# Optimization experiments

Hardware: AMD Instinct MI355X
Metric: run time of the kernel (lower is better)

## Reference

```python
import jax, jax.numpy as jnp
import numpy as np

ALPHA_LEAKY = 0.2
EPS = 1e-10


def setup_inputs() -> dict:
    key = jax.random.key(0)
    ks = jax.random.split(key, 7)
    Nq, Nk, E, D = 100000, 100000, 1600000, 64
    return {
        "query_nodes": jax.random.normal(ks[0], (Nq, D), dtype=jnp.float32),
        "key_value_nodes": jax.random.normal(ks[1], (Nk, D), dtype=jnp.float32),
        "edge_index": jax.random.randint(ks[2], (2, E), 0, Nq, dtype=jnp.int64),
        "proj_w": jax.random.normal(ks[3], (D, D), dtype=jnp.float32) * 0.1,
        "proj_b": jax.random.normal(ks[4], (D,), dtype=jnp.float32) * 0.1,
        "attend_w": jax.random.normal(ks[5], (1, 2 * D), dtype=jnp.float32) * 0.1,
        "attend_b": jax.random.normal(ks[6], (1,), dtype=jnp.float32) * 0.1,
    }


def reference(query_nodes, key_value_nodes, edge_index, proj_w, proj_b, attend_w, attend_b):
    Nq, D = query_nodes.shape
    qi, ki = edge_index[0], edge_index[1]  # [E], [E]
    # per-edge gathered + projected features (torch Linear: x @ W.T + b)
    query_proj = query_nodes[qi] @ proj_w.T + proj_b      # [E, D]
    kv_proj = key_value_nodes[ki] @ proj_w.T + proj_b     # [E, D]
    # attend(concat([qp, kp])) == qp @ Wq.T + kp @ Wk.T + b  (avoids [E,2D] concat)
    wq, wk = attend_w[:, :D], attend_w[:, D:]
    e = query_proj @ wq[0] + kv_proj @ wk[0] + attend_b[0]  # [E]
    e = jax.nn.leaky_relu(e, negative_slope=ALPHA_LEAKY)
    # segment-wise (per query node) numerically-stable softmax
    e_max = jax.ops.segment_max(e, qi, num_segments=Nq)    # [Nq] (-inf for empty)
    e_exp = jnp.exp(e - e_max[qi])                          # [E]
    e_sum = jax.ops.segment_sum(e_exp, qi, num_segments=Nq)  # [Nq]
    attention = e_exp / (e_sum[qi] + EPS)                   # [E]  (dropout = identity in eval)
    # weighted scatter-add aggregation back to query nodes
    weighted_values = kv_proj * attention[:, None]          # [E, D]
    aggregated_context = jax.ops.segment_sum(weighted_values, qi, num_segments=Nq)  # [Nq, D]
    return aggregated_context
```

## Files before the change

### kernel.cpp

```cpp
#include <hip/hip_runtime.h>

#define ALPHA_LEAKY 0.2f
#define EPS_F 1e-10f

#define BSHIFT 7
#define BRANGE 128
#define NBMAX 1024
#define CHUNK_B 16384
#define KBUF_CAP 3072
#define GC_STRIDE 16

using half4_t = __attribute__((ext_vector_type(4))) _Float16;
using f32x4 = __attribute__((ext_vector_type(4))) float;

__device__ __forceinline__ unsigned short f2bf(float x) {
  unsigned int u = __float_as_uint(x);
  return (unsigned short)((u + 0x7fffu + ((u >> 16) & 1u)) >> 16);
}

__global__ __launch_bounds__(1024) void bin_kernel(
    const int* __restrict__ eq, const int* __restrict__ ek,
    int* __restrict__ gcursor, unsigned int* __restrict__ pairs, int E,
    int NB) {
  __shared__ int lcnt[NBMAX];
  __shared__ int lbase[NBMAX];
  const int t = threadIdx.x;
  for (int i = t; i < NBMAX; i += 1024) lcnt[i] = 0;
  __syncthreads();

  const int cbase = blockIdx.x * CHUNK_B;
  int4 qv[4], kv[4];
#pragma unroll
  for (int j = 0; j < 4; ++j) {
    const int e0 = cbase + (((j << 10) + t) << 2);
    if (e0 + 3 < E) {
      qv[j] = *(const int4*)(eq + e0);
      kv[j] = *(const int4*)(ek + e0);
    } else {
      int tq[4] = {-1, -1, -1, -1}, tk[4] = {0, 0, 0, 0};
      for (int r = 0; r < 4; ++r)
        if (e0 + r < E) { tq[r] = eq[e0 + r]; tk[r] = ek[e0 + r]; }
      qv[j] = make_int4(tq[0], tq[1], tq[2], tq[3]);
      kv[j] = make_int4(tk[0], tk[1], tk[2], tk[3]);
    }
    if (qv[j].x >= 0) atomicAdd(&lcnt[qv[j].x >> BSHIFT], 1);
    if (qv[j].y >= 0) atomicAdd(&lcnt[qv[j].y >> BSHIFT], 1);
    if (qv[j].z >= 0) atomicAdd(&lcnt[qv[j].z >> BSHIFT], 1);
    if (qv[j].w >= 0) atomicAdd(&lcnt[qv[j].w >> BSHIFT], 1);
  }
  __syncthreads();
  for (int i = t; i < NB; i += 1024) {
    lbase[i] = lcnt[i] ? atomicAdd(&gcursor[i * GC_STRIDE], lcnt[i]) : 0;
    lcnt[i] = 0;
  }
  __syncthreads();
#pragma unroll
  for (int j = 0; j < 4; ++j) {
    const int qs[4] = {qv[j].x, qv[j].y, qv[j].z, qv[j].w};
    const int ks[4] = {kv[j].x, kv[j].y, kv[j].z, kv[j].w};
#pragma unroll
    for (int r = 0; r < 4; ++r) {
      if (qs[r] >= 0) {
        const int b = qs[r] >> BSHIFT;
        const int idx = lbase[b] + atomicAdd(&lcnt[b], 1);
        if (idx < KBUF_CAP)
          pairs[(size_t)b * KBUF_CAP + idx] =
              ((unsigned int)(qs[r] & (BRANGE - 1)) << 20) |
              (unsigned int)ks[r];
      }
    }
  }
}

__global__ __launch_bounds__(256) void proj_kernel(
    const float* __restrict__ qnodes, const float* __restrict__ kvnodes,
    const float* __restrict__ W, const float* __restrict__ pb,
    const float* __restrict__ aw, unsigned int* __restrict__ Kp16,
    float* __restrict__ sq, float* __restrict__ sk,
    int Nq, int Nk, int projBlocks) {
  const int t = threadIdx.x;
  __shared__ float pt0[256];
  __shared__ __align__(16) float us[64];
  __shared__ float cq_s;
  const int lane = t & 63;
  const int waveId = blockIdx.x * 4 + (t >> 6);
  const int nWaves = projBlocks * 4;

  {
    const int pd = t & 63, og = t >> 6;
    float s0 = 0.f;
#pragma unroll
    for (int oo = 0; oo < 16; ++oo) {
      const int o = og * 16 + oo;
      s0 = fmaf(aw[o], W[o * 64 + pd], s0);
    }
    pt0[t] = s0;
  }
  __syncthreads();
  if (t < 64) {
    us[t] = (pt0[t] + pt0[t + 64]) + (pt0[t + 128] + pt0[t + 192]);
    if (t == 0) {
      float c0 = 0.f;
      for (int o = 0; o < 64; ++o) c0 = fmaf(aw[o], pb[o], c0);
      cq_s = c0;
    }
  }
  __syncthreads();

  {
    const int sub = lane & 15, ng = lane >> 4;
    const float4 uv = ((const float4*)us)[sub];
    const float c = cq_s;
    for (int base = waveId * 4; base < Nq; base += nWaves * 4) {
      const int n = base + ng;
      float s = 0.f;
      if (n < Nq) {
        const float4 x = *(const float4*)(qnodes + (size_t)n * 64 + sub * 4);
        s = x.x * uv.x + x.y * uv.y + x.z * uv.z + x.w * uv.w;
      }
#pragma unroll
      for (int off = 1; off <= 8; off <<= 1) s += __shfl_xor(s, off, 64);
      if (sub == 0 && n < Nq) sq[n] = s + c;
    }
  }

  const int c = lane & 15, g = lane >> 4;

  half4_t Bf[4][4];
  float pbv[4];
#pragma unroll
  for (int nt = 0; nt < 4; ++nt) {
    pbv[nt] = pb[nt * 16 + c];
#pragma unroll
    for (int ks = 0; ks < 4; ++ks) {
      const float4 wv =
          *(const float4*)(W + (size_t)(nt * 16 + c) * 64 + ks * 16 + g * 4);
      half4_t h;
      h[0] = (_Float16)wv.x;
      h[1] = (_Float16)wv.y;
      h[2] = (_Float16)wv.z;
      h[3] = (_Float16)wv.w;
      Bf[nt][ks] = h;
    }
  }
  const float a0 = aw[64 + c], a1 = aw[80 + c], a2 = aw[96 + c],
              a3 = aw[112 + c];

  const int ntiles = (Nk + 15) >> 4;
  for (int tile = waveId; tile < ntiles; tile += nWaves) {
    const int n0 = tile << 4;
    const int arow = n0 + c;
    const bool aok = arow < Nk;
    const float* xr = kvnodes + (size_t)arow * 64 + g * 4;

    half4_t Af[4];
#pragma unroll
    for (int ks = 0; ks < 4; ++ks) {
      const float4 xv =
          aok ? *(const float4*)(xr + ks * 16) : make_float4(0.f, 0.f, 0.f, 0.f);
      half4_t h;
      h[0] = (_Float16)xv.x;
      h[1] = (_Float16)xv.y;
      h[2] = (_Float16)xv.z;
      h[3] = (_Float16)xv.w;
      Af[ks] = h;
    }

    f32x4 acc0 = {pbv[0], pbv[0], pbv[0], pbv[0]};
    f32x4 acc1 = {pbv[1], pbv[1], pbv[1], pbv[1]};
    f32x4 acc2 = {pbv[2], pbv[2], pbv[2], pbv[2]};
    f32x4 acc3 = {pbv[3], pbv[3], pbv[3], pbv[3]};
#pragma unroll
    for (int ks = 0; ks < 4; ++ks) {
      acc0 = __builtin_amdgcn_mfma_f32_16x16x16f16(Af[ks], Bf[0][ks], acc0, 0, 0, 0);
      acc1 = __builtin_amdgcn_mfma_f32_16x16x16f16(Af[ks], Bf[1][ks], acc1, 0, 0, 0);
      acc2 = __builtin_amdgcn_mfma_f32_16x16x16f16(Af[ks], Bf[2][ks], acc2, 0, 0, 0);
      acc3 = __builtin_amdgcn_mfma_f32_16x16x16f16(Af[ks], Bf[3][ks], acc3, 0, 0, 0);
    }

#pragma unroll
    for (int r = 0; r < 4; ++r) {
      const int node = n0 + g * 4 + r;
      if (node < Nk) {
        const unsigned int u0 =
            ((unsigned int)f2bf(acc1[r]) << 16) | f2bf(acc0[r]);
        const unsigned int u1 =
            ((unsigned int)f2bf(acc3[r]) << 16) | f2bf(acc2[r]);
        unsigned int* kp = Kp16 + (size_t)node * 32;
        kp[c] = u0;
        kp[16 + c] = u1;
      }
    }

    float ws0 = acc0[0] * a0 + acc1[0] * a1 + acc2[0] * a2 + acc3[0] * a3;
    float ws1 = acc0[1] * a0 + acc1[1] * a1 + acc2[1] * a2 + acc3[1] * a3;
    float ws2 = acc0[2] * a0 + acc1[2] * a1 + acc2[2] * a2 + acc3[2] * a3;
    float ws3 = acc0[3] * a0 + acc1[3] * a1 + acc2[3] * a2 + acc3[3] * a3;
#pragma unroll
    for (int off = 1; off <= 8; off <<= 1) {
      ws0 += __shfl_xor(ws0, off, 64);
      ws1 += __shfl_xor(ws1, off, 64);
      ws2 += __shfl_xor(ws2, off, 64);
      ws3 += __shfl_xor(ws3, off, 64);
    }
    if (c == 0) {
      const int nb4 = n0 + g * 4;
      if (nb4 + 3 < Nk) {
        *(float4*)(sk + nb4) = make_float4(ws0, ws1, ws2, ws3);
      } else {
        if (nb4 + 0 < Nk) sk[nb4 + 0] = ws0;
        if (nb4 + 1 < Nk) sk[nb4 + 1] = ws1;
        if (nb4 + 2 < Nk) sk[nb4 + 2] = ws2;
        if (nb4 + 3 < Nk) sk[nb4 + 3] = ws3;
      }
    }
  }
}

__global__ __launch_bounds__(512, 6) void sort_agg_kernel(
    const unsigned int* __restrict__ pairs, const int* __restrict__ gcursor,
    const float* __restrict__ sq, const float* __restrict__ sk,
    const float* __restrict__ ab, const unsigned int* __restrict__ Kp16,
    float* __restrict__ out, int Nq) {
  __shared__ int lcnt[BRANGE];
  __shared__ int lcur[BRANGE];
  __shared__ int lstart[BRANGE + 1];
  __shared__ int kibuf[KBUF_CAP];
  __shared__ int wso2[2];

  const int t = threadIdx.x;
  const int b = blockIdx.x;
  const int qlo = b << BSHIFT;
  int n = gcursor[b * GC_STRIDE];
  if (n > KBUF_CAP) n = KBUF_CAP;
  const size_t base = (size_t)b * KBUF_CAP;

  if (t < BRANGE) lcnt[t] = 0;
  __syncthreads();

  unsigned int pv[6];
  int np = 0;
#pragma unroll
  for (int r = 0; r < 6; ++r) {
    const int i = t + (r << 9);
    if (i < n) { pv[r] = pairs[base + i]; ++np; }
  }
#pragma unroll
  for (int r = 0; r < 6; ++r)
    if (r < np) atomicAdd(&lcnt[pv[r] >> 20], 1);
  __syncthreads();

  const int lane = t & 63, wv = t >> 6;
  int v = 0, x = 0;
  if (t < BRANGE) {
    v = lcnt[t];
    x = v;
#pragma unroll
    for (int off = 1; off < 64; off <<= 1) {
      const int y = __shfl_up(x, off, 64);
      if (lane >= off) x += y;
    }
    if (lane == 63) wso2[wv] = x;
  }
  __syncthreads();
  if (t < BRANGE) {
    const int excl = ((wv == 1) ? wso2[0] : 0) + x - v;
    lstart[t] = excl;
    lcur[t] = excl;
    if (t == BRANGE - 1) lstart[BRANGE] = excl + v;
  }
  __syncthreads();

#pragma unroll
  for (int r = 0; r < 6; ++r)
    if (r < np)
      kibuf[atomicAdd(&lcur[pv[r] >> 20], 1)] = (int)(pv[r] & 0xFFFFFu);
  __syncthreads();

  const int ng = lane >> 3, dg = lane & 7;
  const float abv = ab[0];
#pragma unroll
  for (int pass = 0; pass < 2; ++pass) {
    const int l = (pass << 6) + (wv << 3) + ng;
    const int node = qlo + l;
    const bool act = node < Nq;
    const int s = act ? lstart[l] : 0;
    const int e = act ? lstart[l + 1] : 0;
    const float sqn = act ? sq[node] + abv : 0.f;

    float acc[8] = {0.f, 0.f, 0.f, 0.f, 0.f, 0.f, 0.f, 0.f};
    float wsum = 0.f;
    const int jm = e - 1;
#pragma unroll 1
    for (int j = s; j < e; j += 4) {
      const int ka = kibuf[j];
      const int kb = kibuf[min(j + 1, jm)];
      const int kc = kibuf[min(j + 2, jm)];
      const int kd = kibuf[min(j + 3, jm)];
      const float ea = sk[ka];
      const float eb = sk[kb];
      const float ec = sk[kc];
      const float ed = sk[kd];
      const uint4 ua = *(const uint4*)(Kp16 + (size_t)ka * 32 + (dg << 2));
      const uint4 ub = *(const uint4*)(Kp16 + (size_t)kb * 32 + (dg << 2));
      const uint4 uc = *(const uint4*)(Kp16 + (size_t)kc * 32 + (dg << 2));
      const uint4 ud = *(const uint4*)(Kp16 + (size_t)kd * 32 + (dg << 2));

      float xa = sqn + ea; xa = xa > 0.f ? xa : ALPHA_LEAKY * xa;
      float xb = sqn + eb; xb = xb > 0.f ? xb : ALPHA_LEAKY * xb;
      float xc = sqn + ec; xc = xc > 0.f ? xc : ALPHA_LEAKY * xc;
      float xd = sqn + ed; xd = xd > 0.f ? xd : ALPHA_LEAKY * xd;
      const float wa = __expf(xa);
      const float wb = (j + 1 < e) ? __expf(xb) : 0.f;
      const float wc = (j + 2 < e) ? __expf(xc) : 0.f;
      const float wd = (j + 3 < e) ? __expf(xd) : 0.f;

#define ACC8(W, U)                                             \
  acc[0] = fmaf(W, __uint_as_float(U.x << 16), acc[0]);        \
  acc[1] = fmaf(W, __uint_as_float(U.x & 0xffff0000u), acc[1]);\
  acc[2] = fmaf(W, __uint_as_float(U.y << 16), acc[2]);        \
  acc[3] = fmaf(W, __uint_as_float(U.y & 0xffff0000u), acc[3]);\
  acc[4] = fmaf(W, __uint_as_float(U.z << 16), acc[4]);        \
  acc[5] = fmaf(W, __uint_as_float(U.z & 0xffff0000u), acc[5]);\
  acc[6] = fmaf(W, __uint_as_float(U.w << 16), acc[6]);        \
  acc[7] = fmaf(W, __uint_as_float(U.w & 0xffff0000u), acc[7]);
      ACC8(wa, ua)
      ACC8(wb, ub)
      ACC8(wc, uc)
      ACC8(wd, ud)
#undef ACC8
      wsum += (wa + wb) + (wc + wd);
    }

    if (act) {
      const float inv = 1.0f / (wsum + EPS_F);
      const int obase = ((dg & 3) << 2) + ((dg >> 2) << 5);
      float4 r0 = {acc[0] * inv, acc[2] * inv, acc[4] * inv, acc[6] * inv};
      float4 r1 = {acc[1] * inv, acc[3] * inv, acc[5] * inv, acc[7] * inv};
      float* o = out + (size_t)node * 64 + obase;
      *(float4*)o = r0;
      *(float4*)(o + 16) = r1;
    }
  }
}

extern "C" void kernel_launch(void* const* d_in, const int* in_sizes, int n_in,
                              void* d_out, int out_size, void* d_ws, size_t ws_size,
                              hipStream_t stream) {
  const float* qnodes = (const float*)d_in[0];
  const float* kvnodes = (const float*)d_in[1];
  const int* ei = (const int*)d_in[2];
  const float* W = (const float*)d_in[3];
  const float* pb = (const float*)d_in[4];
  const float* aw = (const float*)d_in[5];
  const float* ab = (const float*)d_in[6];

  const int Nq = in_sizes[0] / 64;
  const int Nk = in_sizes[1] / 64;
  const int E = in_sizes[2] / 2;
  const int NB = (Nq + BRANGE - 1) >> BSHIFT;

  const int* eq = ei;
  const int* ek = ei + E;

  char* ws = (char*)d_ws;
  unsigned int* pairs = (unsigned int*)ws;
  unsigned int* Kp16 = pairs + (size_t)NBMAX * KBUF_CAP;
  float* sq = (float*)(Kp16 + (size_t)Nk * 32);
  float* sk = sq + Nq;
  int* gcursor = (int*)(sk + Nk);

  hipMemsetAsync(gcursor, 0, NBMAX * GC_STRIDE * sizeof(int), stream);

  const int binBlocks = (E + CHUNK_B - 1) / CHUNK_B;
  bin_kernel<<<binBlocks, 1024, 0, stream>>>(eq, ek, gcursor, pairs, E, NB);

  const int projBlocks = 1664;
  proj_kernel<<<projBlocks, 256, 0, stream>>>(qnodes, kvnodes, W, pb, aw,
                                              Kp16, sq, sk, Nq, Nk,
                                              projBlocks);

  sort_agg_kernel<<<NB, 512, 0, stream>>>(pairs, gcursor, sq, sk, ab, Kp16,
                                          (float*)d_out, Nq);
}
```

Measured before the change: 185.1 us.

## Fuse bin and proj kernels, split aggregation into two blocks per bucket

Merges the edge-binning kernel and the node-projection kernel into one launch, where some blocks bin edges and the rest run the projection with 1024-thread blocks. This removes a launch boundary and lets the two independent stages overlap. The aggregation kernel now launches two blocks per bucket, one per half of the 128 query nodes. That doubles parallelism but repeats the local counting sort of the pairs in both blocks. The inner gather loop is also unrolled to 8 edges to keep more loads in flight.

```diff
diff --git a/kernel.cpp b/kernel.cpp
--- a/kernel.cpp
+++ b/kernel.cpp
@@ -18,87 +18,92 @@
   return (unsigned short)((u + 0x7fffu + ((u >> 16) & 1u)) >> 16);
 }
 
-__global__ __launch_bounds__(1024) void bin_kernel(
+__global__ __launch_bounds__(1024) void bin_proj_kernel(
     const int* __restrict__ eq, const int* __restrict__ ek,
     int* __restrict__ gcursor, unsigned int* __restrict__ pairs, int E,
-    int NB) {
-  __shared__ int lcnt[NBMAX];
-  __shared__ int lbase[NBMAX];
-  const int t = threadIdx.x;
-  for (int i = t; i < NBMAX; i += 1024) lcnt[i] = 0;
-  __syncthreads();
-
-  const int cbase = blockIdx.x * CHUNK_B;
-  int4 qv[4], kv[4];
-#pragma unroll
-  for (int j = 0; j < 4; ++j) {
-    const int e0 = cbase + (((j << 10) + t) << 2);
-    if (e0 + 3 < E) {
-      qv[j] = *(const int4*)(eq + e0);
-      kv[j] = *(const int4*)(ek + e0);
-    } else {
-      int tq[4] = {-1, -1, -1, -1}, tk[4] = {0, 0, 0, 0};
-      for (int r = 0; r < 4; ++r)
-        if (e0 + r < E) { tq[r] = eq[e0 + r]; tk[r] = ek[e0 + r]; }
-      qv[j] = make_int4(tq[0], tq[1], tq[2], tq[3]);
-      kv[j] = make_int4(tk[0], tk[1], tk[2], tk[3]);
-    }
-    if (qv[j].x >= 0) atomicAdd(&lcnt[qv[j].x >> BSHIFT], 1);
-    if (qv[j].y >= 0) atomicAdd(&lcnt[qv[j].y >> BSHIFT], 1);
-    if (qv[j].z >= 0) atomicAdd(&lcnt[qv[j].z >> BSHIFT], 1);
-    if (qv[j].w >= 0) atomicAdd(&lcnt[qv[j].w >> BSHIFT], 1);
-  }
-  __syncthreads();
-  for (int i = t; i < NB; i += 1024) {
-    lbase[i] = lcnt[i] ? atomicAdd(&gcursor[i * GC_STRIDE], lcnt[i]) : 0;
-    lcnt[i] = 0;
-  }
-  __syncthreads();
-#pragma unroll
-  for (int j = 0; j < 4; ++j) {
-    const int qs[4] = {qv[j].x, qv[j].y, qv[j].z, qv[j].w};
-    const int ks[4] = {kv[j].x, kv[j].y, kv[j].z, kv[j].w};
-#pragma unroll
-    for (int r = 0; r < 4; ++r) {
-      if (qs[r] >= 0) {
-        const int b = qs[r] >> BSHIFT;
-        const int idx = lbase[b] + atomicAdd(&lcnt[b], 1);
-        if (idx < KBUF_CAP)
-          pairs[(size_t)b * KBUF_CAP + idx] =
-              ((unsigned int)(qs[r] & (BRANGE - 1)) << 20) |
-              (unsigned int)ks[r];
-      }
-    }
-  }
-}
-
-__global__ __launch_bounds__(256) void proj_kernel(
+    int NB, int binBlocks,
     const float* __restrict__ qnodes, const float* __restrict__ kvnodes,
     const float* __restrict__ W, const float* __restrict__ pb,
     const float* __restrict__ aw, unsigned int* __restrict__ Kp16,
     float* __restrict__ sq, float* __restrict__ sk,
     int Nq, int Nk, int projBlocks) {
   const int t = threadIdx.x;
-  __shared__ float pt0[256];
+
+  if (blockIdx.x < binBlocks) {
+    __shared__ int lcnt[NBMAX];
+    __shared__ int lbase[NBMAX];
+    for (int i = t; i < NBMAX; i += 1024) lcnt[i] = 0;
+    __syncthreads();
+
+    const int cbase = blockIdx.x * CHUNK_B;
+    int4 qv[4], kv[4];
+#pragma unroll
+    for (int j = 0; j < 4; ++j) {
+      const int e0 = cbase + (((j << 10) + t) << 2);
+      if (e0 + 3 < E) {
+        qv[j] = *(const int4*)(eq + e0);
+        kv[j] = *(const int4*)(ek + e0);
+      } else {
+        int tq[4] = {-1, -1, -1, -1}, tk[4] = {0, 0, 0, 0};
+        for (int r = 0; r < 4; ++r)
+          if (e0 + r < E) { tq[r] = eq[e0 + r]; tk[r] = ek[e0 + r]; }
+        qv[j] = make_int4(tq[0], tq[1], tq[2], tq[3]);
+        kv[j] = make_int4(tk[0], tk[1], tk[2], tk[3]);
+      }
+      if (qv[j].x >= 0) atomicAdd(&lcnt[qv[j].x >> BSHIFT], 1);
+      if (qv[j].y >= 0) atomicAdd(&lcnt[qv[j].y >> BSHIFT], 1);
+      if (qv[j].z >= 0) atomicAdd(&lcnt[qv[j].z >> BSHIFT], 1);
+      if (qv[j].w >= 0) atomicAdd(&lcnt[qv[j].w >> BSHIFT], 1);
+    }
+    __syncthreads();
+    for (int i = t; i < NB; i += 1024) {
+      lbase[i] = lcnt[i] ? atomicAdd(&gcursor[i * GC_STRIDE], lcnt[i]) : 0;
+      lcnt[i] = 0;
+    }
+    __syncthreads();
+#pragma unroll
+    for (int j = 0; j < 4; ++j) {
+      const int qs[4] = {qv[j].x, qv[j].y, qv[j].z, qv[j].w};
+      const int ks[4] = {kv[j].x, kv[j].y, kv[j].z, kv[j].w};
+#pragma unroll
+      for (int r = 0; r < 4; ++r) {
+        if (qs[r] >= 0) {
+          const int b = qs[r] >> BSHIFT;
+          const int idx = lbase[b] + atomicAdd(&lcnt[b], 1);
+          if (idx < KBUF_CAP)
+            pairs[(size_t)b * KBUF_CAP + idx] =
+                ((unsigned int)(qs[r] & (BRANGE - 1)) << 20) |
+                (unsigned int)ks[r];
+        }
+      }
+    }
+    return;
+  }
+
+  __shared__ float pt0[1024];
   __shared__ __align__(16) float us[64];
   __shared__ float cq_s;
   const int lane = t & 63;
-  const int waveId = blockIdx.x * 4 + (t >> 6);
-  const int nWaves = projBlocks * 4;
+  const int projId = blockIdx.x - binBlocks;
+  const int waveId = projId * 16 + (t >> 6);
+  const int nWaves = projBlocks * 16;
 
   {
     const int pd = t & 63, og = t >> 6;
     float s0 = 0.f;
 #pragma unroll
-    for (int oo = 0; oo < 16; ++oo) {
-      const int o = og * 16 + oo;
+    for (int oo = 0; oo < 4; ++oo) {
+      const int o = og * 4 + oo;
       s0 = fmaf(aw[o], W[o * 64 + pd], s0);
     }
     pt0[t] = s0;
   }
   __syncthreads();
   if (t < 64) {
-    us[t] = (pt0[t] + pt0[t + 64]) + (pt0[t + 128] + pt0[t + 192]);
+    float s = 0.f;
+#pragma unroll
+    for (int g2 = 0; g2 < 16; ++g2) s += pt0[g2 * 64 + t];
+    us[t] = s;
     if (t == 0) {
       float c0 = 0.f;
       for (int o = 0; o < 64; ++o) c0 = fmaf(aw[o], pb[o], c0);
@@ -229,7 +234,8 @@
   __shared__ int wso2[2];
 
   const int t = threadIdx.x;
-  const int b = blockIdx.x;
+  const int b = blockIdx.x >> 1;
+  const int pass = blockIdx.x & 1;
   const int qlo = b << BSHIFT;
   int n = gcursor[b * GC_STRIDE];
   if (n > KBUF_CAP) n = KBUF_CAP;
@@ -279,8 +285,7 @@
 
   const int ng = lane >> 3, dg = lane & 7;
   const float abv = ab[0];
-#pragma unroll
-  for (int pass = 0; pass < 2; ++pass) {
+  {
     const int l = (pass << 6) + (wv << 3) + ng;
     const int node = qlo + l;
     const bool act = node < Nq;
@@ -290,30 +295,6 @@
 
     float acc[8] = {0.f, 0.f, 0.f, 0.f, 0.f, 0.f, 0.f, 0.f};
     float wsum = 0.f;
-    const int jm = e - 1;
-#pragma unroll 1
-    for (int j = s; j < e; j += 4) {
-      const int ka = kibuf[j];
-      const int kb = kibuf[min(j + 1, jm)];
-      const int kc = kibuf[min(j + 2, jm)];
-      const int kd = kibuf[min(j + 3, jm)];
-      const float ea = sk[ka];
-      const float eb = sk[kb];
-      const float ec = sk[kc];
-      const float ed = sk[kd];
-      const uint4 ua = *(const uint4*)(Kp16 + (size_t)ka * 32 + (dg << 2));
-      const uint4 ub = *(const uint4*)(Kp16 + (size_t)kb * 32 + (dg << 2));
-      const uint4 uc = *(const uint4*)(Kp16 + (size_t)kc * 32 + (dg << 2));
-      const uint4 ud = *(const uint4*)(Kp16 + (size_t)kd * 32 + (dg << 2));
-
-      float xa = sqn + ea; xa = xa > 0.f ? xa : ALPHA_LEAKY * xa;
-      float xb = sqn + eb; xb = xb > 0.f ? xb : ALPHA_LEAKY * xb;
-      float xc = sqn + ec; xc = xc > 0.f ? xc : ALPHA_LEAKY * xc;
-      float xd = sqn + ed; xd = xd > 0.f ? xd : ALPHA_LEAKY * xd;
-      const float wa = __expf(xa);
-      const float wb = (j + 1 < e) ? __expf(xb) : 0.f;
-      const float wc = (j + 2 < e) ? __expf(xc) : 0.f;
-      const float wd = (j + 3 < e) ? __expf(xd) : 0.f;
 
 #define ACC8(W, U)                                             \
   acc[0] = fmaf(W, __uint_as_float(U.x << 16), acc[0]);        \
@@ -324,13 +305,66 @@
   acc[5] = fmaf(W, __uint_as_float(U.z & 0xffff0000u), acc[5]);\
   acc[6] = fmaf(W, __uint_as_float(U.w << 16), acc[6]);        \
   acc[7] = fmaf(W, __uint_as_float(U.w & 0xffff0000u), acc[7]);
-      ACC8(wa, ua)
-      ACC8(wb, ub)
-      ACC8(wc, uc)
-      ACC8(wd, ud)
+
+    int j = s;
+    for (; j + 8 <= e; j += 8) {
+      const int k0 = kibuf[j + 0], k1 = kibuf[j + 1];
+      const int k2 = kibuf[j + 2], k3 = kibuf[j + 3];
+      const int k4 = kibuf[j + 4], k5 = kibuf[j + 5];
+      const int k6 = kibuf[j + 6], k7 = kibuf[j + 7];
+      const float e0 = sk[k0], e1 = sk[k1], e2 = sk[k2], e3 = sk[k3];
+      const float e4 = sk[k4], e5 = sk[k5], e6 = sk[k6], e7 = sk[k7];
+      const uint4 u0 = *(const uint4*)(Kp16 + (size_t)k0 * 32 + (dg << 2));
+      const uint4 u1 = *(const uint4*)(Kp16 + (size_t)k1 * 32 + (dg << 2));
+      const uint4 u2 = *(const uint4*)(Kp16 + (size_t)k2 * 32 + (dg << 2));
+      const uint4 u3 = *(const uint4*)(Kp16 + (size_t)k3 * 32 + (dg << 2));
+      const uint4 u4 = *(const uint4*)(Kp16 + (size_t)k4 * 32 + (dg << 2));
+      const uint4 u5 = *(const uint4*)(Kp16 + (size_t)k5 * 32 + (dg << 2));
+      const uint4 u6 = *(const uint4*)(Kp16 + (size_t)k6 * 32 + (dg << 2));
+      const uint4 u7 = *(const uint4*)(Kp16 + (size_t)k7 * 32 + (dg << 2));
+
+      float x0 = sqn + e0; x0 = x0 > 0.f ? x0 : ALPHA_LEAKY * x0;
+      float x1 = sqn + e1; x1 = x1 > 0.f ? x1 : ALPHA_LEAKY * x1;
+      float x2 = sqn + e2; x2 = x2 > 0.f ? x2 : ALPHA_LEAKY * x2;
+      float x3 = sqn + e3; x3 = x3 > 0.f ? x3 : ALPHA_LEAKY * x3;
+      float x4 = sqn + e4; x4 = x4 > 0.f ? x4 : ALPHA_LEAKY * x4;
+      float x5 = sqn + e5; x5 = x5 > 0.f ? x5 : ALPHA_LEAKY * x5;
+      float x6 = sqn + e6; x6 = x6 > 0.f ? x6 : ALPHA_LEAKY * x6;
+      float x7 = sqn + e7; x7 = x7 > 0.f ? x7 : ALPHA_LEAKY * x7;
+      const float w0 = __expf(x0), w1 = __expf(x1);
+      const float w2 = __expf(x2), w3 = __expf(x3);
+      const float w4 = __expf(x4), w5 = __expf(x5);
+      const float w6 = __expf(x6), w7 = __expf(x7);
+
+      ACC8(w0, u0) ACC8(w1, u1) ACC8(w2, u2) ACC8(w3, u3)
+      ACC8(w4, u4) ACC8(w5, u5) ACC8(w6, u6) ACC8(w7, u7)
+      wsum += ((w0 + w1) + (w2 + w3)) + ((w4 + w5) + (w6 + w7));
+    }
+    const int jm = e - 1;
+    for (; j < e; j += 4) {
+      const int ka = kibuf[j];
+      const int kb = kibuf[min(j + 1, jm)];
+      const int kc = kibuf[min(j + 2, jm)];
+      const int kd = kibuf[min(j + 3, jm)];
+      const float ea = sk[ka], eb = sk[kb], ec = sk[kc], ed = sk[kd];
+      const uint4 ua = *(const uint4*)(Kp16 + (size_t)ka * 32 + (dg << 2));
+      const uint4 ub = *(const uint4*)(Kp16 + (size_t)kb * 32 + (dg << 2));
+      const uint4 uc = *(const uint4*)(Kp16 + (size_t)kc * 32 + (dg << 2));
+      const uint4 ud = *(const uint4*)(Kp16 + (size_t)kd * 32 + (dg << 2));
+
+      float xa = sqn + ea; xa = xa > 0.f ? xa : ALPHA_LEAKY * xa;
+      float xb = sqn + eb; xb = xb > 0.f ? xb : ALPHA_LEAKY * xb;
+      float xc = sqn + ec; xc = xc > 0.f ? xc : ALPHA_LEAKY * xc;
+      float xd = sqn + ed; xd = xd > 0.f ? xd : ALPHA_LEAKY * xd;
+      const float wa = __expf(xa);
+      const float wb = (j + 1 < e) ? __expf(xb) : 0.f;
+      const float wc = (j + 2 < e) ? __expf(xc) : 0.f;
+      const float wd = (j + 3 < e) ? __expf(xd) : 0.f;
+
+      ACC8(wa, ua) ACC8(wb, ub) ACC8(wc, uc) ACC8(wd, ud)
+      wsum += (wa + wb) + (wc + wd);
+    }
 #undef ACC8
-      wsum += (wa + wb) + (wc + wd);
-    }
 
     if (act) {
       const float inv = 1.0f / (wsum + EPS_F);
@@ -373,13 +407,11 @@
   hipMemsetAsync(gcursor, 0, NBMAX * GC_STRIDE * sizeof(int), stream);
 
   const int binBlocks = (E + CHUNK_B - 1) / CHUNK_B;
-  bin_kernel<<<binBlocks, 1024, 0, stream>>>(eq, ek, gcursor, pairs, E, NB);
-
-  const int projBlocks = 1664;
-  proj_kernel<<<projBlocks, 256, 0, stream>>>(qnodes, kvnodes, W, pb, aw,
-                                              Kp16, sq, sk, Nq, Nk,
-                                              projBlocks);
-
-  sort_agg_kernel<<<NB, 512, 0, stream>>>(pairs, gcursor, sq, sk, ab, Kp16,
-                                          (float*)d_out, Nq);
+  const int projBlocks = 512 - binBlocks;
+  bin_proj_kernel<<<binBlocks + projBlocks, 1024, 0, stream>>>(
+      eq, ek, gcursor, pairs, E, NB, binBlocks, qnodes, kvnodes, W, pb, aw,
+      Kp16, sq, sk, Nq, Nk, projBlocks);
+
+  sort_agg_kernel<<<NB * 2, 512, 0, stream>>>(pairs, gcursor, sq, sk, ab,
+                                              Kp16, (float*)d_out, Nq);
 }
```

Result: faster. 168.3 us (-9.1%).
